# Kernel tuning notes

Measured on AMD Instinct MI355X. Metric: run time of the kernel, lower is better.

## Reference

```python
import jax, jax.numpy as jnp
from jax import lax
import numpy as np

B, C, H, W = 8, 256, 64, 64
DSTATE, DCONV, EXPAND = 16, 4, 2
DI = EXPAND * C          # 512 d_inner
DTR = (C + 15) // 16     # 16 dt_rank = ceil(d_model/16)

# ---------- helpers ----------

def _ln(x, g, b):
    m = x.mean(-1, keepdims=True)
    v = x.var(-1, keepdims=True)
    return (x - m) * lax.rsqrt(v + 1e-5) * g + b


def _bn(x, g, b):  # BatchNorm2d, training-mode batch stats
    m = x.mean((0, 2, 3), keepdims=True)
    v = x.var((0, 2, 3), keepdims=True)
    return (x - m) * lax.rsqrt(v + 1e-5) * g[None, :, None, None] + b[None, :, None, None]


def _gn(x, g, b, groups=32):
    Bb, Cc, Hh, Ww = x.shape
    xr = x.reshape(Bb, groups, Cc // groups, Hh, Ww)
    m = xr.mean((2, 3, 4), keepdims=True)
    v = xr.var((2, 3, 4), keepdims=True)
    xr = (xr - m) * lax.rsqrt(v + 1e-5)
    return xr.reshape(Bb, Cc, Hh, Ww) * g[None, :, None, None] + b[None, :, None, None]


def _hsig(x):  # h_sigmoid: relu6(x+3)/6
    return jnp.clip(x + 3.0, 0.0, 6.0) / 6.0


def _axial(v, idx, pos):
    # v: [B,C,N]; pos: [1,C,16] linearly resized to N (align_corners=False == half-pixel)
    N = v.shape[-1]
    pe = jax.image.resize(pos, (1, pos.shape[1], N), method='linear')
    return v + pe + idx  # idx interpolation is identity (same size)


def _dwconvT(x, w):
    # ConvTranspose2d(k=3, stride=2, pad=1, out_pad=1, groups=C) == lhs-dilated corr with flipped kernel
    wf = w[:, :, ::-1, ::-1]
    return lax.conv_general_dilated(x, wf, window_strides=(1, 1), padding=((1, 2), (1, 2)),
                                    lhs_dilation=(2, 2), dimension_numbers=('NCHW', 'OIHW', 'NCHW'),
                                    feature_group_count=x.shape[1])


def _mamba(h, in_w, conv_w, conv_b, xproj_w, dt_w, dt_b, Alog, Dp, out_w):
    # standard mamba_ssm Mamba block forward; h: [B,L,d_model]
    Bb, L, _ = h.shape
    di = in_w.shape[0] // 2
    N = Alog.shape[1]
    dtr = dt_w.shape[1]
    xz = h @ in_w.T                      # [B,L,2*di]
    xm, zg = xz[..., :di], xz[..., di:]
    # causal depthwise conv1d (pad K-1 left == torch pad both + slice [:L])
    xc = lax.conv_general_dilated(xm.transpose(0, 2, 1), conv_w, (1,), [(conv_w.shape[2] - 1, 0)],
                                  dimension_numbers=('NCH', 'OIH', 'NCH'), feature_group_count=di)
    u = jax.nn.silu(xc + conv_b[None, :, None]).transpose(0, 2, 1)  # [B,L,di]
    dbl = u @ xproj_w.T                  # [B,L,dtr+2N]
    dt = jax.nn.softplus(dbl[..., :dtr] @ dt_w.T + dt_b)            # [B,L,di]
    Bm = dbl[..., dtr:dtr + N]
    Cm = dbl[..., dtr + N:]
    A = -jnp.exp(Alog)                   # [di,N]
    dA = jnp.exp(dt[..., None] * A)      # [B,L,di,N]
    dBu = (dt * u)[..., None] * Bm[:, :, None, :]

    def step(hst, inp):
        dA_t, dBu_t = inp
        hst = dA_t * hst + dBu_t
        return hst, hst

    h0 = jnp.zeros((Bb, di, N), dt.dtype)
    _, hs = lax.scan(step, h0, (dA.transpose(1, 0, 2, 3), dBu.transpose(1, 0, 2, 3)))
    y = jnp.einsum('lbdn,bln->bld', hs, Cm) + Dp * u
    y = y * jax.nn.silu(zg)
    return y @ out_w.T


def _forward(x, pos_embed, ln_w, ln_b, proj_w, proj_b,
             up_dw_w, up_bn1_g, up_bn1_b, up_pw_w, up_bn2_g, up_bn2_b,
             down_pw_w, down_bn_g, down_bn_b, gn_g, gn_b,
             f_in_w, f_conv_w, f_conv_b, f_xproj_w, f_dt_w, f_dt_b, f_Alog, f_D, f_out_w,
             b_in_w, b_conv_w, b_conv_b, b_xproj_w, b_dt_w, b_dt_b, b_Alog, b_D, b_out_w):
    # upsample branch: dwconvT -> BN -> ReLU -> 1x1 -> BN -> ReLU6
    z = _dwconvT(x, up_dw_w)
    z = jax.nn.relu(_bn(z, up_bn1_g, up_bn1_b))
    z = jnp.einsum('oc,bchw->bohw', up_pw_w, z)
    z = jnp.clip(_bn(z, up_bn2_g, up_bn2_b), 0.0, 6.0)  # act1 = ReLU6
    dt = x.dtype
    col_max = _ln(_axial(x.max(2), jnp.argmax(x, 2).astype(dt), pos_embed).transpose(0, 2, 1), ln_w, ln_b)
    col_min = _ln(_axial(x.min(2), jnp.argmin(x, 2).astype(dt), pos_embed).transpose(0, 2, 1), ln_w, ln_b)
    row_max = _ln(_axial(x.max(3), jnp.argmax(x, 3).astype(dt), pos_embed).transpose(0, 2, 1), ln_w, ln_b)
    row_min = _ln(_axial(x.min(3), jnp.argmin(x, 3).astype(dt), pos_embed).transpose(0, 2, 1), ln_w, ln_b)
    result_max = jnp.concatenate([col_max, row_max], 1)  # [B, W+H, C]
    result_min = jnp.concatenate([col_min, row_min], 1)
    fpar = (f_in_w, f_conv_w, f_conv_b, f_xproj_w, f_dt_w, f_dt_b, f_Alog, f_D, f_out_w)
    bpar = (b_in_w, b_conv_w, b_conv_b, b_xproj_w, b_dt_w, b_dt_b, b_Alog, b_D, b_out_w)
    fmax = _ln(_mamba(result_max, *fpar), ln_w, ln_b)
    fmin = _ln(_mamba(result_min, *fpar), ln_w, ln_b)
    bmax = _ln(_mamba(jnp.flip(result_max, 1), *bpar), ln_w, ln_b)
    bmin = _ln(_mamba(jnp.flip(result_min, 1), *bpar), ln_w, ln_b)
    res_max = jnp.concatenate([fmax, jnp.flip(bmax, 1)], -1) @ proj_w.T + proj_b
    res_max = _ln(res_max, ln_w, ln_b)
    res_min = jnp.concatenate([fmin, jnp.flip(bmin, 1)], -1) @ proj_w.T + proj_b
    res_min = _ln(res_min, ln_w, ln_b)
    res = res_max[:, :, None, :] + res_min[:, None, :, :]  # [B,L,L,C], L=H+W
    res = res.transpose(0, 3, 1, 2)                        # [B,C,L,L] == [B,C,2H,2W]
    res = _hsig(res) * z
    res = _gn(res, gn_g, gn_b)
    res = jnp.einsum('oc,bchw->bohw', down_pw_w, res[:, :, ::2, ::2])  # 1x1 stride-2 conv
    res = _bn(res, down_bn_g, down_bn_b)
    res = _gn(res, gn_g, gn_b)
    res = res + x
    res = _gn(res, gn_g, gn_b)
    return res


def setup_inputs() -> dict:
    key = jax.random.key(0)
    ks = jax.random.split(key, 32)

    def n(i, shape, s=0.02):
        return jax.random.normal(ks[i], shape, jnp.float32) * s

    inp = {}
    inp['x'] = jax.random.normal(ks[0], (B, C, H, W), jnp.float32)
    inp['pos_embed'] = jax.random.normal(ks[1], (1, C, 16), jnp.float32)
    inp['ln_w'] = jnp.ones((C,), jnp.float32)
    inp['ln_b'] = jnp.zeros((C,), jnp.float32)
    inp['proj_w'] = n(2, (C, 2 * C))
    inp['proj_b'] = jnp.zeros((C,), jnp.float32)
    inp['up_dw_w'] = n(3, (C, 1, 3, 3), 0.1)
    inp['up_bn1_g'] = jnp.ones((C,), jnp.float32)
    inp['up_bn1_b'] = jnp.zeros((C,), jnp.float32)
    inp['up_pw_w'] = n(4, (C, C), 0.05)
    inp['up_bn2_g'] = jnp.ones((C,), jnp.float32)
    inp['up_bn2_b'] = jnp.zeros((C,), jnp.float32)
    inp['down_pw_w'] = n(5, (C, C), 0.05)
    inp['down_bn_g'] = jnp.ones((C,), jnp.float32)
    inp['down_bn_b'] = jnp.zeros((C,), jnp.float32)
    inp['gn_g'] = jnp.ones((C,), jnp.float32)
    inp['gn_b'] = jnp.zeros((C,), jnp.float32)
    Alog = jnp.tile(jnp.log(jnp.arange(1, DSTATE + 1, dtype=jnp.float32))[None, :], (DI, 1))
    dtb = jnp.full((DI,), float(np.log(np.expm1(0.01))), jnp.float32)
    for p, k0 in (('f', 6), ('b', 16)):
        inp[p + '_in_w'] = n(k0, (2 * DI, C))
        inp[p + '_conv_w'] = n(k0 + 1, (DI, 1, DCONV), 0.2)
        inp[p + '_conv_b'] = jnp.zeros((DI,), jnp.float32)
        inp[p + '_xproj_w'] = n(k0 + 2, (DTR + 2 * DSTATE, DI))
        inp[p + '_dt_w'] = n(k0 + 3, (DI, DTR), 0.1)
        inp[p + '_dt_b'] = dtb
        inp[p + '_Alog'] = Alog
        inp[p + '_D'] = jnp.ones((DI,), jnp.float32)
        inp[p + '_out_w'] = n(k0 + 4, (C, DI))
    return inp


def reference(x, pos_embed, ln_w, ln_b, proj_w, proj_b,
              up_dw_w, up_bn1_g, up_bn1_b, up_pw_w, up_bn2_g, up_bn2_b,
              down_pw_w, down_bn_g, down_bn_b, gn_g, gn_b,
              f_in_w, f_conv_w, f_conv_b, f_xproj_w, f_dt_w, f_dt_b, f_Alog, f_D, f_out_w,
              b_in_w, b_conv_w, b_conv_b, b_xproj_w, b_dt_w, b_dt_b, b_Alog, b_D, b_out_w):
    return _forward(x, pos_embed, ln_w, ln_b, proj_w, proj_b,
                    up_dw_w, up_bn1_g, up_bn1_b, up_pw_w, up_bn2_g, up_bn2_b,
                    down_pw_w, down_bn_g, down_bn_b, gn_g, gn_b,
                    f_in_w, f_conv_w, f_conv_b, f_xproj_w, f_dt_w, f_dt_b, f_Alog, f_D, f_out_w,
                    b_in_w, b_conv_w, b_conv_b, b_xproj_w, b_dt_w, b_dt_b, b_Alog, b_D, b_out_w)
```

## Files before the change

### kernel.cpp

```cpp
#include <hip/hip_runtime.h>
#include <hip/hip_bf16.h>

typedef __hip_bfloat16 bf16;
typedef __attribute__((ext_vector_type(8))) short bf16x8v;
typedef __attribute__((ext_vector_type(4))) short bf16x4v;
typedef __attribute__((ext_vector_type(4))) float f32x4v;

#define B_ 8
#define C_ 256
#define L_ 128
#define MB 1048576UL

__device__ inline float b2f(bf16 v){ return __bfloat162float(v); }
__device__ inline bf16 f2b(float v){ return __float2bfloat16(v); }
__device__ inline short b2s(bf16 v){ return *(short*)&v; }
__device__ inline float siluf(float x){ return x / (1.f + expf(-x)); }
__device__ inline float softplusf(float x){ return (x > 20.f) ? x : log1pf(expf(x)); }
__device__ inline float vclamp(float v){ return fmaxf(v, 0.f) + 1e-5f; }

__device__ inline void bred2(float& a, float& b, float* red){
  #pragma unroll
  for (int m = 1; m < 64; m <<= 1){ a += __shfl_xor(a, m); b += __shfl_xor(b, m); }
  int tid = threadIdx.x, wave = tid >> 6, lane = tid & 63;
  __syncthreads();
  if (lane == 0){ red[wave] = a; red[8 + wave] = b; }
  __syncthreads();
  a = red[0] + red[1] + red[2] + red[3];
  b = red[8] + red[9] + red[10] + red[11];
}

__device__ inline int tswz(int p, int c){
  return (p*512 + c*2) ^ (((p ^ (p >> 2)) & 7) << 4);
}

__global__ __launch_bounds__(64) void pool1_kernel(const float* __restrict__ x, const float* __restrict__ pos,
    float* __restrict__ pcolmax, float* __restrict__ pcolmin,
    float* __restrict__ prowmax, float* __restrict__ prowmin, float* __restrict__ sxb)
{
  int c = blockIdx.x, b = blockIdx.y, t = threadIdx.x;
  __shared__ float xs[64][65];
  const float* xp = x + ((long)(b*C_ + c))*4096;
  for (int i = 0; i < 64; i++) xs[i][t] = xp[i*64 + t];
  __syncthreads();
  float tt = 0.25f*(float)t - 0.375f;
  const float* pp = pos + c*16;
  float pe;
  if (tt <= 0.f) pe = pp[0];
  else if (tt >= 15.f) pe = pp[15];
  else { int f = (int)floorf(tt); float w = tt - (float)f; pe = pp[f]*(1.f - w) + pp[f+1]*w; }
  float vmax = -1e30f, vmin = 1e30f; int amax = 0, amin = 0;
  for (int j = 0; j < 64; j++){
    float v = xs[t][j];
    if (v > vmax){ vmax = v; amax = j; }
    if (v < vmin){ vmin = v; amin = j; }
  }
  long o = (long)(b*64 + t)*C_ + c;
  prowmax[o] = vmax + pe + (float)amax;
  prowmin[o] = vmin + pe + (float)amin;
  vmax = -1e30f; vmin = 1e30f; amax = 0; amin = 0;
  float sx = 0.f, sx2 = 0.f;
  for (int i = 0; i < 64; i++){
    float v = xs[i][t];
    if (v > vmax){ vmax = v; amax = i; }
    if (v < vmin){ vmin = v; amin = i; }
    sx += v; sx2 += v*v;
  }
  pcolmax[o] = vmax + pe + (float)amax;
  pcolmin[o] = vmin + pe + (float)amin;
  #pragma unroll
  for (int m = 1; m < 64; m <<= 1){ sx += __shfl_xor(sx, m); sx2 += __shfl_xor(sx2, m); }
  if (t == 0){ sxb[(b << 8) + c] = sx; sxb[2048 + (b << 8) + c] = sx2; }
}

__global__ __launch_bounds__(256) void pool2_kernel(const float* __restrict__ pcolmax, const float* __restrict__ pcolmin,
    const float* __restrict__ prowmax, const float* __restrict__ prowmin,
    const float* __restrict__ lnw, const float* __restrict__ lnb, bf16* __restrict__ hbuf)
{
  int r = blockIdx.x, b = blockIdx.y, c = threadIdx.x;
  __shared__ float red[16];
  int p = r & 63;
  long src = (long)(b*64 + p)*C_ + c;
  float vmax = (r < 64) ? pcolmax[src] : prowmax[src];
  float vmin = (r < 64) ? pcolmin[src] : prowmin[src];
  float gw = lnw[c], gb = lnb[c];
  long row = (long)b*L_ + r, frow = (long)b*L_ + (127 - r);
  float s = vmax, s2 = vmax*vmax;
  bred2(s, s2, red);
  float m = s*(1.f/256.f), var = s2*(1.f/256.f) - m*m;
  float o = (vmax - m)*rsqrtf(vclamp(var))*gw + gb;
  hbuf[0*262144 + row*C_ + c]  = f2b(o);
  hbuf[2*262144 + frow*C_ + c] = f2b(o);
  s = vmin; s2 = vmin*vmin;
  bred2(s, s2, red);
  m = s*(1.f/256.f); var = s2*(1.f/256.f) - m*m;
  o = (vmin - m)*rsqrtf(vclamp(var))*gw + gb;
  hbuf[1*262144 + row*C_ + c]  = f2b(o);
  hbuf[3*262144 + frow*C_ + c] = f2b(o);
}

__global__ __launch_bounds__(256) void dwz1_kernel(const float* __restrict__ x, const float* __restrict__ dw,
    bf16* __restrict__ z1, float* __restrict__ bn1sum, float* __restrict__ bn1sq)
{
  int bc = blockIdx.x; int c = bc & 255;
  int tid = threadIdx.x;
  __shared__ float xs[4096];
  const float* xp = x + (long)bc*4096;
  for (int it = 0; it < 16; it++) xs[it*256 + tid] = xp[it*256 + tid];
  float w[9];
  #pragma unroll
  for (int q = 0; q < 9; q++) w[q] = dw[c*9 + q];
  __syncthreads();
  bf16* zp = z1 + (long)bc*16384;
  float s = 0.f, s2 = 0.f;
  for (int it = 0; it < 64; it++){
    int p = it*256 + tid; int i = p >> 7, j = p & 127;
    int xi = i >> 1, xj = j >> 1;
    int io = i & 1, jo = j & 1;
    int xi1 = (xi < 63) ? xi + 1 : 63;
    int xj1 = (xj < 63) ? xj + 1 : 63;
    float XA = xs[xi*64 + xj];
    float XB = xs[xi*64 + xj1];
    float XC = xs[xi1*64 + xj];
    float XD = xs[xi1*64 + xj1];
    float wA = jo ? (io ? w[8] : w[5]) : (io ? w[7] : w[4]);
    float wB = (jo && j < 127) ? (io ? w[6] : w[3]) : 0.f;
    float wC = (io && i < 127) ? (jo ? w[2] : w[1]) : 0.f;
    float wD = (io && jo && i < 127 && j < 127) ? w[0] : 0.f;
    float acc = wA*XA;
    acc += wB*XB;
    acc += wC*XC;
    acc += wD*XD;
    zp[p] = f2b(acc);
    s += acc; s2 += acc*acc;
  }
  __shared__ float red[16];
  bred2(s, s2, red);
  if (tid == 0){ atomicAdd(&bn1sum[c], s); atomicAdd(&bn1sq[c], s2); }
}

__global__ __launch_bounds__(256) void wcvt_all_kernel(
    const float* __restrict__ s0, const float* __restrict__ s1, const float* __restrict__ s2,
    const float* __restrict__ s3, const float* __restrict__ s4, const float* __restrict__ s5,
    const float* __restrict__ s6, const float* __restrict__ s7, const float* __restrict__ s8,
    bf16* __restrict__ d0, bf16* __restrict__ d1, bf16* __restrict__ d2,
    bf16* __restrict__ d3, bf16* __restrict__ d4, bf16* __restrict__ d5,
    bf16* __restrict__ d6, bf16* __restrict__ d7, bf16* __restrict__ d8)
{
  int seg = blockIdx.y;
  const float* s; bf16* d; int n;
  switch (seg){
    case 0: s = s0; d = d0; n = 262144; break;
    case 1: s = s1; d = d1; n = 262144; break;
    case 2: s = s2; d = d2; n = 24576;  break;
    case 3: s = s3; d = d3; n = 24576;  break;
    case 4: s = s4; d = d4; n = 131072; break;
    case 5: s = s5; d = d5; n = 131072; break;
    case 6: s = s6; d = d6; n = 131072; break;
    case 7: s = s7; d = d7; n = 65536;  break;
    default: s = s8; d = d8; n = 65536; break;
  }
  long i = ((long)blockIdx.x*256 + threadIdx.x)*4;
  if (i >= n) return;
  float4 v = *(const float4*)&s[i];
  bf16 o[4] = {f2b(v.x), f2b(v.y), f2b(v.z), f2b(v.w)};
  *(uint2*)&d[i] = *(const uint2*)o;
}

__global__ __launch_bounds__(256) void pwz_fused_kernel(const bf16* __restrict__ z1,
    const float* __restrict__ bn1sum, const float* __restrict__ bn1sq,
    const float* __restrict__ g1, const float* __restrict__ b1,
    const bf16* __restrict__ Wb, bf16* __restrict__ z2,
    float* __restrict__ bn2part)
{
  int b = blockIdx.y;
  int p0 = blockIdx.x*64;
  int tid = threadIdx.x;
  __shared__ __align__(16) short Tb[16384];
  {
    int pc = tid & 15, ch = tid >> 4;
    #pragma unroll
    for (int it = 0; it < 8; it++){
      int c = (ch + it*16)*2;
      const bf16* r0 = &z1[((long)(b*C_ + c))*16384 + p0 + pc*4];
      bf16x4v va = *(const bf16x4v*)r0;
      bf16x4v vb = *(const bf16x4v*)(r0 + 16384);
      float m0v = bn1sum[c]*(1.f/131072.f);
      float v0 = bn1sq[c]*(1.f/131072.f) - m0v*m0v;
      float a0 = g1[c]*rsqrtf(vclamp(v0));
      float d0 = b1[c] - m0v*a0;
      float m1v = bn1sum[c+1]*(1.f/131072.f);
      float v1 = bn1sq[c+1]*(1.f/131072.f) - m1v*m1v;
      float a1 = g1[c+1]*rsqrtf(vclamp(v1));
      float d1 = b1[c+1] - m1v*a1;
      #pragma unroll
      for (int k = 0; k < 4; k++){
        int p = pc*4 + k;
        bf16 h0; *(short*)&h0 = va[k];
        bf16 h1; *(short*)&h1 = vb[k];
        bf16 o0 = f2b(fmaxf(b2f(h0)*a0 + d0, 0.f));
        bf16 o1 = f2b(fmaxf(b2f(h1)*a1 + d1, 0.f));
        unsigned int u = ((unsigned int)(*(unsigned short*)&o1) << 16) | (unsigned int)(*(unsigned short*)&o0);
        *(unsigned int*)((char*)Tb + tswz(p, c)) = u;
      }
    }
  }
  __syncthreads();
  int wave = tid >> 6, lane = tid & 63;
  int quad = lane >> 4, l16 = lane & 15;
  f32x4v acc[4][4];
  #pragma unroll
  for (int i = 0; i < 4; i++)
    #pragma unroll
    for (int j = 0; j < 4; j++) acc[i][j] = (f32x4v){0.f, 0.f, 0.f, 0.f};
  for (int k0 = 0; k0 < 256; k0 += 32){
    int c = k0 + quad*8;
    bf16x8v a[4], bb[4];
    #pragma unroll
    for (int ms = 0; ms < 4; ms++)
      a[ms] = *(const bf16x8v*)&Wb[(wave*64 + ms*16 + l16)*C_ + c];
    #pragma unroll
    for (int ns = 0; ns < 4; ns++){
      int p = ns*16 + l16;
      bb[ns] = *(const bf16x8v*)((const char*)Tb + tswz(p, c));
    }
    #pragma unroll
    for (int ms = 0; ms < 4; ms++)
      #pragma unroll
      for (int ns = 0; ns < 4; ns++)
        acc[ms][ns] = __builtin_amdgcn_mfma_f32_16x16x32_bf16(bb[ns], a[ms], acc[ms][ns], 0, 0, 0);
  }
  int slot = (blockIdx.x & 7) | (b << 3);
  #pragma unroll
  for (int ms = 0; ms < 4; ms++){
    int o = wave*64 + ms*16 + l16;
    long rowbase = ((long)(b*C_ + o))*16384 + p0;
    float s = 0.f, s2 = 0.f;
    #pragma unroll
    for (int ns = 0; ns < 4; ns++){
      bf16 ov[4];
      #pragma unroll
      for (int r = 0; r < 4; r++){
        bf16 bv = f2b(acc[ms][ns][r]);
        ov[r] = bv;
        float vv = b2f(bv);
        s += vv; s2 += vv*vv;
      }
      *(uint2*)&z2[rowbase + ns*16 + quad*4] = *(const uint2*)ov;
    }
    s += __shfl_xor(s, 16);  s += __shfl_xor(s, 32);
    s2 += __shfl_xor(s2, 16); s2 += __shfl_xor(s2, 32);
    if (quad == 0){
      atomicAdd(&bn2part[slot*256 + o], s);
      atomicAdd(&bn2part[16384 + slot*256 + o], s2);
    }
  }
}

__global__ __launch_bounds__(256) void inproj_mfma_kernel(const bf16* __restrict__ hb,
    const bf16* __restrict__ Wif, const bf16* __restrict__ Wib2, bf16* __restrict__ xz)
{
  int v = blockIdx.z;
  int m0 = blockIdx.y*256, n0 = blockIdx.x*64;
  const bf16* A = hb + (long)v*262144;
  const bf16* W = (v >= 2) ? Wib2 : Wif;
  bf16* out = xz + (long)v*1048576;
  int tid = threadIdx.x;
  int wave = tid >> 6, lane = tid & 63;
  int quad = lane >> 4, l16 = lane & 15;
  f32x4v acc[4][4];
  #pragma unroll
  for (int i = 0; i < 4; i++)
    #pragma unroll
    for (int j = 0; j < 4; j++) acc[i][j] = (f32x4v){0.f, 0.f, 0.f, 0.f};
  for (int k0 = 0; k0 < 256; k0 += 32){
    int c = k0 + quad*8;
    bf16x8v a[4], bb[4];
    #pragma unroll
    for (int ms = 0; ms < 4; ms++)
      a[ms] = *(const bf16x8v*)&A[(long)(m0 + wave*64 + ms*16 + l16)*256 + c];
    #pragma unroll
    for (int ns = 0; ns < 4; ns++)
      bb[ns] = *(const bf16x8v*)&W[(long)(n0 + ns*16 + l16)*256 + c];
    #pragma unroll
    for (int ms = 0; ms < 4; ms++)
      #pragma unroll
      for (int ns = 0; ns < 4; ns++)
        acc[ms][ns] = __builtin_amdgcn_mfma_f32_16x16x32_bf16(bb[ns], a[ms], acc[ms][ns], 0, 0, 0);
  }
  #pragma unroll
  for (int ms = 0; ms < 4; ms++){
    int m = m0 + wave*64 + ms*16 + l16;
    #pragma unroll
    for (int ns = 0; ns < 4; ns++){
      bf16 ov[4];
      #pragma unroll
      for (int r = 0; r < 4; r++) ov[r] = f2b(acc[ms][ns][r]);
      *(uint2*)&out[(long)m*1024 + n0 + ns*16 + quad*4] = *(const uint2*)ov;
    }
  }
}

__global__ __launch_bounds__(256) void xproj_mfma_kernel(const bf16* __restrict__ ub,
    const bf16* __restrict__ Wxf, const bf16* __restrict__ Wxb, float* __restrict__ dblb)
{
  int v = blockIdx.y;
  int m0 = blockIdx.x*256;
  const bf16* A = ub + (long)v*524288;
  const bf16* W = (v >= 2) ? Wxb : Wxf;
  float* out = dblb + (long)v*49152;
  int tid = threadIdx.x;
  int wave = tid >> 6, lane = tid & 63;
  int quad = lane >> 4, l16 = lane & 15;
  f32x4v acc[4][3];
  #pragma unroll
  for (int i = 0; i < 4; i++)
    #pragma unroll
    for (int j = 0; j < 3; j++) acc[i][j] = (f32x4v){0.f, 0.f, 0.f, 0.f};
  for (int k0 = 0; k0 < 512; k0 += 32){
    int c = k0 + quad*8;
    bf16x8v a[4], bb[3];
    #pragma unroll
    for (int ms = 0; ms < 4; ms++)
      a[ms] = *(const bf16x8v*)&A[(long)(m0 + wave*64 + ms*16 + l16)*512 + c];
    #pragma unroll
    for (int ns = 0; ns < 3; ns++)
      bb[ns] = *(const bf16x8v*)&W[(long)(ns*16 + l16)*512 + c];
    #pragma unroll
    for (int ms = 0; ms < 4; ms++)
      #pragma unroll
      for (int ns = 0; ns < 3; ns++)
        acc[ms][ns] = __builtin_amdgcn_mfma_f32_16x16x32_bf16(bb[ns], a[ms], acc[ms][ns], 0, 0, 0);
  }
  #pragma unroll
  for (int ms = 0; ms < 4; ms++){
    int m = m0 + wave*64 + ms*16 + l16;
    #pragma unroll
    for (int ns = 0; ns < 3; ns++)
      *(f32x4v*)&out[(long)m*48 + ns*16 + quad*4] = acc[ms][ns];
  }
}

__global__ __launch_bounds__(256) void outproj_mfma_kernel(const bf16* __restrict__ yb,
    const bf16* __restrict__ Wof, const bf16* __restrict__ Wob, float* __restrict__ mo)
{
  int v = blockIdx.z;
  int m0 = blockIdx.y*256, n0 = blockIdx.x*64;
  const bf16* A = yb + (long)v*524288;
  const bf16* W = (v >= 2) ? Wob : Wof;
  float* out = mo + (long)v*262144;
  int tid = threadIdx.x;
  int wave = tid >> 6, lane = tid & 63;
  int quad = lane >> 4, l16 = lane & 15;
  f32x4v acc[4][4];
  #pragma unroll
  for (int i = 0; i < 4; i++)
    #pragma unroll
    for (int j = 0; j < 4; j++) acc[i][j] = (f32x4v){0.f, 0.f, 0.f, 0.f};
  for (int k0 = 0; k0 < 512; k0 += 32){
    int c = k0 + quad*8;
    bf16x8v a[4], bb[4];
    #pragma unroll
    for (int ms = 0; ms < 4; ms++)
      a[ms] = *(const bf16x8v*)&A[(long)(m0 + wave*64 + ms*16 + l16)*512 + c];
    #pragma unroll
    for (int ns = 0; ns < 4; ns++)
      bb[ns] = *(const bf16x8v*)&W[(long)(n0 + ns*16 + l16)*512 + c];
    #pragma unroll
    for (int ms = 0; ms < 4; ms++)
      #pragma unroll
      for (int ns = 0; ns < 4; ns++)
        acc[ms][ns] = __builtin_amdgcn_mfma_f32_16x16x32_bf16(bb[ns], a[ms], acc[ms][ns], 0, 0, 0);
  }
  #pragma unroll
  for (int ms = 0; ms < 4; ms++){
    int m = m0 + wave*64 + ms*16 + l16;
    #pragma unroll
    for (int ns = 0; ns < 4; ns++)
      *(f32x4v*)&out[(long)m*256 + n0 + ns*16 + quad*4] = acc[ms][ns];
  }
}

__global__ __launch_bounds__(256) void pj_mfma_kernel(const bf16* __restrict__ cb,
    const bf16* __restrict__ Wp, const float* __restrict__ pb, float* __restrict__ rp)
{
  int z = blockIdx.z;
  int m0 = blockIdx.y*256, n0 = blockIdx.x*64;
  const bf16* A = cb + (long)z*524288;
  float* out = rp + (long)z*262144;
  int tid = threadIdx.x;
  int wave = tid >> 6, lane = tid & 63;
  int quad = lane >> 4, l16 = lane & 15;
  f32x4v acc[4][4];
  #pragma unroll
  for (int i = 0; i < 4; i++)
    #pragma unroll
    for (int j = 0; j < 4; j++) acc[i][j] = (f32x4v){0.f, 0.f, 0.f, 0.f};
  for (int k0 = 0; k0 < 512; k0 += 32){
    int c = k0 + quad*8;
    bf16x8v a[4], bb[4];
    #pragma unroll
    for (int ms = 0; ms < 4; ms++)
      a[ms] = *(const bf16x8v*)&A[(long)(m0 + wave*64 + ms*16 + l16)*512 + c];
    #pragma unroll
    for (int ns = 0; ns < 4; ns++)
      bb[ns] = *(const bf16x8v*)&Wp[(long)(n0 + ns*16 + l16)*512 + c];
    #pragma unroll
    for (int ms = 0; ms < 4; ms++)
      #pragma unroll
      for (int ns = 0; ns < 4; ns++)
        acc[ms][ns] = __builtin_amdgcn_mfma_f32_16x16x32_bf16(bb[ns], a[ms], acc[ms][ns], 0, 0, 0);
  }
  #pragma unroll
  for (int ns = 0; ns < 4; ns++){
    float4 pbv = *(const float4*)&pb[n0 + ns*16 + quad*4];
    #pragma unroll
    for (int ms = 0; ms < 4; ms++){
      int m = m0 + wave*64 + ms*16 + l16;
      f32x4v vv = acc[ms][ns];
      vv[0] += pbv.x; vv[1] += pbv.y; vv[2] += pbv.z; vv[3] += pbv.w;
      *(f32x4v*)&out[(long)m*256 + n0 + ns*16 + quad*4] = vv;
    }
  }
}

__global__ __launch_bounds__(256) void gemm_kernel(
  const float* __restrict__ Abase, long sA, int lda,
  const float* __restrict__ W0, const float* __restrict__ W1,
  const float* __restrict__ bias0, const float* __restrict__ bias1, int wsplit,
  float* __restrict__ Cbase, long sC, int ldc,
  int M, int N, int K, int act)
{
  int z = blockIdx.z;
  const float* A = Abase + (long)z*sA;
  float* Cp = Cbase + (long)z*sC;
  const float* W = (z >= wsplit) ? W1 : W0;
  const float* bias = (z >= wsplit) ? bias1 : bias0;
  int m0 = blockIdx.y*64, n0 = blockIdx.x*64;
  __shared__ __align__(16) float As[16][68];
  __shared__ __align__(16) float Ws[16][68];
  int tid = threadIdx.x, tx = tid & 15, ty = tid >> 4;
  float acc[4][4] = {};
  for (int k0 = 0; k0 < K; k0 += 16){
    #pragma unroll
    for (int q = 0; q < 4; q++){
      int e = tid + q*256; int r = e >> 4, kk = e & 15;
      int mi = m0 + r, ki = k0 + kk;
      As[kk][r] = (mi < M && ki < K) ? A[(long)mi*lda + ki] : 0.f;
    }
    #pragma unroll
    for (int q = 0; q < 4; q++){
      int e = tid + q*256; int n = e >> 4, kk = e & 15;
      int ni = n0 + n, ki = k0 + kk;
      Ws[kk][n] = (ni < N && ki < K) ? W[(long)ni*K + ki] : 0.f;
    }
    __syncthreads();
    #pragma unroll
    for (int kk = 0; kk < 16; kk++){
      float4 a4 = *(const float4*)&As[kk][ty*4];
      float4 b4 = *(const float4*)&Ws[kk][tx*4];
      float av[4] = {a4.x, a4.y, a4.z, a4.w};
      float bv[4] = {b4.x, b4.y, b4.z, b4.w};
      #pragma unroll
      for (int mm = 0; mm < 4; mm++)
        #pragma unroll
        for (int nn = 0; nn < 4; nn++) acc[mm][nn] += av[mm]*bv[nn];
    }
    __syncthreads();
  }
  #pragma unroll
  for (int mm = 0; mm < 4; mm++){
    int mi = m0 + ty*4 + mm;
    if (mi >= M) continue;
    #pragma unroll
    for (int nn = 0; nn < 4; nn++){
      int ni = n0 + tx*4 + nn;
      if (ni >= N) continue;
      float v = acc[mm][nn];
      if (bias) v += bias[ni];
      if (act == 2) v = softplusf(v);
      Cp[(long)mi*ldc + ni] = v;
    }
  }
}

__global__ __launch_bounds__(512) void conv1d_kernel(const bf16* __restrict__ xzb,
    const float* __restrict__ fw, const float* __restrict__ fb,
    const float* __restrict__ bw, const float* __restrict__ bb,
    bf16* __restrict__ ub)
{
  int l = blockIdx.x, b = blockIdx.y, v = blockIdx.z, d = threadIdx.x;
  const bf16* xm = xzb + (long)v*1024*1024;
  const float* w  = (v < 2) ? fw : bw;
  const float* cb = (v < 2) ? fb : bb;
  float acc = cb[d];
  #pragma unroll
  for (int k = 0; k < 4; k++){
    int ll = l - 3 + k;
    if (ll >= 0) acc += b2f(xm[(long)(b*L_ + ll)*1024 + d]) * w[d*4 + k];
  }
  ub[(long)v*1024*512 + (long)(b*L_ + l)*512 + d] = f2b(siluf(acc));
}

__global__ __launch_bounds__(64) void scan_kernel(const float* __restrict__ dtb, const bf16* __restrict__ ub,
    const float* __restrict__ dblb, const bf16* __restrict__ xzb,
    const float* __restrict__ fAlog, const float* __restrict__ fD,
    const float* __restrict__ bAlog, const float* __restrict__ bD,
    bf16* __restrict__ yb)
{
  int v = blockIdx.z, b = blockIdx.y;
  int tid = threadIdx.x;
  int dd = tid & 15, qtr = tid >> 4;
  int d0 = blockIdx.x*16;
  int d = d0 + dd;
  const float* dt  = dtb  + (long)v*1024*512;
  const bf16*  u   = ub   + (long)v*1024*512;
  const float* dbl = dblb + (long)v*1024*48;
  const bf16*  zg  = xzb  + (long)v*1024*1024 + 512;
  const float* Alog = (v < 2) ? fAlog : bAlog;
  const float* Dp   = (v < 2) ? fD : bD;
  __shared__ __align__(16) short sdt[16][136];
  __shared__ __align__(16) short su_[16][136];
  __shared__ __align__(16) short szg[16][136];
  __shared__ __align__(16) short sB [16][136];
  __shared__ __align__(16) short sC [16][136];
  long row = (long)b*L_;
  for (int idx = tid; idx < 2048; idx += 64){
    int l = idx >> 4, j = idx & 15;
    sdt[j][l] = b2s(f2b(dt[(row + l)*512 + d0 + j]));
    su_[j][l] = b2s(u[(row + l)*512 + d0 + j]);
    szg[j][l] = b2s(zg[(row + l)*1024 + d0 + j]);
    sB [j][l] = b2s(f2b(dbl[(row + l)*48 + 16 + j]));
    sC [j][l] = b2s(f2b(dbl[(row + l)*48 + 32 + j]));
  }
  float a2[4];
  #pragma unroll
  for (int n = 0; n < 4; n++) a2[n] = -expf(Alog[d*16 + qtr*4 + n]) * 1.44269504f;
  float Dv = Dp[d];
  float h[4];
  #pragma unroll
  for (int n = 0; n < 4; n++) h[n] = 0.f;
  __syncthreads();
  bf16* yo = yb + (long)v*1024*512;
  for (int l0 = 0; l0 < 128; l0 += 8){
    bf16x8v dt8 = *(const bf16x8v*)&sdt[dd][l0];
    bf16x8v u8  = *(const bf16x8v*)&su_[dd][l0];
    bf16x8v zg8 = *(const bf16x8v*)&szg[dd][l0];
    bf16x8v B8[4], C8[4];
    #pragma unroll
    for (int n = 0; n < 4; n++){
      B8[n] = *(const bf16x8v*)&sB[qtr*4 + n][l0];
      C8[n] = *(const bf16x8v*)&sC[qtr*4 + n][l0];
    }
    #pragma unroll
    for (int k = 0; k < 8; k++){
      bf16 t0; *(short*)&t0 = dt8[k]; float dtv = b2f(t0);
      bf16 t1; *(short*)&t1 = u8[k];  float uv  = b2f(t1);
      bf16 t2; *(short*)&t2 = zg8[k]; float zgv = b2f(t2);
      float dtu = dtv*uv;
      float acc = 0.f;
      #pragma unroll
      for (int n = 0; n < 4; n++){
        float dA = exp2f(dtv*a2[n]);
        bf16 tb; *(short*)&tb = B8[n][k];
        bf16 tc; *(short*)&tc = C8[n][k];
        h[n] = dA*h[n] + dtu*b2f(tb);
        acc += h[n]*b2f(tc);
      }
      acc += __shfl_xor(acc, 16);
      acc += __shfl_xor(acc, 32);
      if (qtr == 0)
        yo[(row + l0 + k)*512 + d] = f2b((acc + Dv*uv) * siluf(zgv));
    }
  }
}

__global__ __launch_bounds__(256) void ln_kernel(const float* __restrict__ inb, bf16* __restrict__ outb0,
    bf16* __restrict__ outb1, float* __restrict__ outf,
    const float* __restrict__ lnw, const float* __restrict__ lnb, int mode)
{
  int r = blockIdx.x, b = blockIdx.y, v = blockIdx.z, c = threadIdx.x;
  long row = (long)b*L_ + r;
  float val = inb[((long)v*1024 + row)*C_ + c];
  __shared__ float red[16];
  float s = val, s2 = val*val;
  bred2(s, s2, red);
  float m = s*(1.f/256.f), var = s2*(1.f/256.f) - m*m;
  float o = (val - m)*rsqrtf(vclamp(var))*lnw[c] + lnb[c];
  if (mode == 1){
    long frow = (long)b*L_ + (127 - r);
    if (v == 0)      outb0[row*512 + c] = f2b(o);
    else if (v == 1) outb1[row*512 + c] = f2b(o);
    else if (v == 2) outb0[frow*512 + 256 + c] = f2b(o);
    else             outb1[frow*512 + 256 + c] = f2b(o);
  } else {
    outf[((long)v*1024 + row)*C_ + c] = o;
  }
}

__global__ __launch_bounds__(256) void hsig_kernel(bf16* __restrict__ z2, const float* __restrict__ rm,
    const float* __restrict__ rn, const float* __restrict__ bn2part,
    const float* __restrict__ g2, const float* __restrict__ b2,
    float* __restrict__ gnsum, float* __restrict__ gnsq)
{
  int c = blockIdx.x, b = blockIdx.y, tid = threadIdx.x;
  __shared__ float red[16];
  __shared__ float rms[128], rns[128];
  if (tid < 128){
    rms[tid] = rm[(long)(b*L_ + tid)*C_ + c];
    rns[tid] = rn[(long)(b*L_ + tid)*C_ + c];
  }
  float pa = 0.f, pb = 0.f;
  if (tid < 64){ pa = bn2part[tid*256 + c]; pb = bn2part[16384 + tid*256 + c]; }
  bred2(pa, pb, red);
  float mm2 = pa*(1.f/131072.f);
  float vv2 = pb*(1.f/131072.f) - mm2*mm2;
  float aa = g2[c] * rsqrtf(vclamp(vv2));
  float dd = b2[c] - mm2*aa;
  bf16* zp = z2 + ((long)(b*C_ + c))*16384;
  float pre[16];
  #pragma unroll
  for (int g = 0; g < 4; g++)
    #pragma unroll
    for (int q = 0; q < 4; q++)
      pre[g*4 + q] = b2f(zp[g*1024 + q*256 + tid]);
  __syncthreads();
  float s = 0.f, s2 = 0.f;
  #pragma unroll
  for (int g = 0; g < 4; g++){
    #pragma unroll
    for (int q = 0; q < 4; q++){
      int p = g*1024 + q*256 + tid; int i = p >> 7, j = p & 127;
      float zv = pre[g*4 + q]*aa + dd;
      zv = fminf(fmaxf(zv, 0.f), 6.f);
      float gate = rms[i] + rns[j];
      gate = fminf(fmaxf(gate + 3.f, 0.f), 6.f) * (1.f/6.f);
      float t = gate*zv;
      s += t; s2 += t*t;
      if (((i | j) & 1) == 0) zp[(i >> 1)*64 + (j >> 1)] = f2b(t);
    }
  }
  for (int g = 4; g < 16; g++){
    #pragma unroll
    for (int q = 0; q < 4; q++){
      int p = g*1024 + q*256 + tid; int i = p >> 7, j = p & 127;
      float zv = b2f(zp[p])*aa + dd;
      zv = fminf(fmaxf(zv, 0.f), 6.f);
      float gate = rms[i] + rns[j];
      gate = fminf(fmaxf(gate + 3.f, 0.f), 6.f) * (1.f/6.f);
      float t = gate*zv;
      s += t; s2 += t*t;
      if (((i | j) & 1) == 0) zp[(i >> 1)*64 + (j >> 1)] = f2b(t);
    }
  }
  bred2(s, s2, red);
  if (tid == 0){ atomicAdd(&gnsum[b*32 + (c >> 3)], s); atomicAdd(&gnsq[b*32 + (c >> 3)], s2); }
}

__global__ __launch_bounds__(256) void pwdown_fused_kernel(const bf16* __restrict__ z2,
    const float* __restrict__ gnsum, const float* __restrict__ gnsq,
    const float* __restrict__ gn_g, const float* __restrict__ gn_b,
    const bf16* __restrict__ Wb, const float* __restrict__ x,
    float* __restrict__ out, float* __restrict__ sds)
{
  int b = blockIdx.y;
  int p0 = blockIdx.x*64;
  int tid = threadIdx.x;
  __shared__ __align__(16) short Tb[16384];
  {
    int pc = tid & 15, ch = tid >> 4;
    #pragma unroll
    for (int it = 0; it < 8; it++){
      int c = (ch + it*16)*2;
      const bf16* r0 = &z2[((long)(b*C_ + c))*16384 + p0 + pc*4];
      bf16x4v va = *(const bf16x4v*)r0;
      bf16x4v vb = *(const bf16x4v*)(r0 + 16384);
      float m0v = gnsum[b*32 + (c >> 3)]*(1.f/131072.f);
      float v0 = gnsq[b*32 + (c >> 3)]*(1.f/131072.f) - m0v*m0v;
      float iv = rsqrtf(vclamp(v0));
      float a0 = iv*gn_g[c],   d0 = gn_b[c]   - m0v*(iv*gn_g[c]);
      float a1 = iv*gn_g[c+1], d1 = gn_b[c+1] - m0v*(iv*gn_g[c+1]);
      #pragma unroll
      for (int k = 0; k < 4; k++){
        int p = pc*4 + k;
        bf16 h0; *(short*)&h0 = va[k];
        bf16 h1; *(short*)&h1 = vb[k];
        bf16 o0 = f2b(b2f(h0)*a0 + d0);
        bf16 o1 = f2b(b2f(h1)*a1 + d1);
        unsigned int u = ((unsigned int)(*(unsigned short*)&o1) << 16) | (unsigned int)(*(unsigned short*)&o0);
        *(unsigned int*)((char*)Tb + tswz(p, c)) = u;
      }
    }
  }
  __syncthreads();
  int wave = tid >> 6, lane = tid & 63;
  int quad = lane >> 4, l16 = lane & 15;
  f32x4v acc[4][4];
  #pragma unroll
  for (int i = 0; i < 4; i++)
    #pragma unroll
    for (int j = 0; j < 4; j++) acc[i][j] = (f32x4v){0.f, 0.f, 0.f, 0.f};
  for (int k0 = 0; k0 < 256; k0 += 32){
    int c = k0 + quad*8;
    bf16x8v a[4], bb[4];
    #pragma unroll
    for (int ms = 0; ms < 4; ms++)
      a[ms] = *(const bf16x8v*)&Wb[(wave*64 + ms*16 + l16)*C_ + c];
    #pragma unroll
    for (int ns = 0; ns < 4; ns++){
      int p = ns*16 + l16;
      bb[ns] = *(const bf16x8v*)((const char*)Tb + tswz(p, c));
    }
    #pragma unroll
    for (int ms = 0; ms < 4; ms++)
      #pragma unroll
      for (int ns = 0; ns < 4; ns++)
        acc[ms][ns] = __builtin_amdgcn_mfma_f32_16x16x32_bf16(bb[ns], a[ms], acc[ms][ns], 0, 0, 0);
  }
  #pragma unroll
  for (int ms = 0; ms < 4; ms++){
    int o = wave*64 + ms*16 + l16;
    long rowbase = ((long)(b*C_ + o))*4096 + p0;
    float sd = 0.f, sd2 = 0.f, sdx = 0.f;
    #pragma unroll
    for (int ns = 0; ns < 4; ns++){
      f32x4v v4 = acc[ms][ns];
      long base = rowbase + ns*16 + quad*4;
      *(f32x4v*)&out[base] = v4;
      float4 xv = *(const float4*)&x[base];
      sd += v4[0] + v4[1] + v4[2] + v4[3];
      sd2 += v4[0]*v4[0] + v4[1]*v4[1] + v4[2]*v4[2] + v4[3]*v4[3];
      sdx += v4[0]*xv.x + v4[1]*xv.y + v4[2]*xv.z + v4[3]*xv.w;
    }
    sd += __shfl_xor(sd, 16);  sd += __shfl_xor(sd, 32);
    sd2 += __shfl_xor(sd2, 16); sd2 += __shfl_xor(sd2, 32);
    sdx += __shfl_xor(sdx, 16); sdx += __shfl_xor(sdx, 32);
    if (quad == 0){
      int oc = (b << 8) + o;
      atomicAdd(&sds[oc], sd);
      atomicAdd(&sds[2048 + oc], sd2);
      atomicAdd(&sds[4096 + oc], sdx);
    }
  }
}

__global__ __launch_bounds__(256) void final_kernel(const float* __restrict__ x,
    const float* __restrict__ sds, const float* __restrict__ sxb,
    const float* __restrict__ dbn_g, const float* __restrict__ dbn_b,
    const float* __restrict__ gn_g, const float* __restrict__ gn_b,
    float* __restrict__ out)
{
  int c = blockIdx.x, b = blockIdx.y, tid = threadIdx.x;
  __shared__ float lv[11][8];
  int g8 = (c >> 3) << 3;
  if (tid < 8){
    int cc = g8 + tid;
    float sd = 0.f, sd2 = 0.f;
    for (int bb2 = 0; bb2 < 8; bb2++){ sd += sds[bb2*256 + cc]; sd2 += sds[2048 + bb2*256 + cc]; }
    float mB = sd*(1.f/32768.f);
    float vB = sd2*(1.f/32768.f) - mB*mB;
    float ab = dbn_g[cc] * rsqrtf(vclamp(vB));
    float db = dbn_b[cc] - mB*ab;
    float inv_n = 1.f/4096.f;
    float m = sds[b*256 + cc]*inv_n, Ed2 = sds[2048 + b*256 + cc]*inv_n;
    float mx = sxb[b*256 + cc]*inv_n, Ex2 = sxb[2048 + b*256 + cc]*inv_n;
    float Edx = sds[4096 + b*256 + cc]*inv_n;
    float Ev = ab*m + db;
    float Ev2 = ab*ab*Ed2 + 2.f*ab*db*m + db*db;
    lv[0][tid] = ab; lv[1][tid] = db; lv[2][tid] = m; lv[3][tid] = Ed2;
    lv[4][tid] = mx; lv[5][tid] = Ex2; lv[6][tid] = Edx; lv[7][tid] = Ev; lv[8][tid] = Ev2;
  }
  __syncthreads();
  if (tid < 8){
    float m1 = 0.f, q1 = 0.f;
    for (int k = 0; k < 8; k++){ m1 += lv[7][k]; q1 += lv[8][k]; }
    m1 *= 0.125f; q1 *= 0.125f;
    int cc = g8 + tid;
    float inv1 = rsqrtf(vclamp(q1 - m1*m1));
    float A1 = inv1*gn_g[cc];
    float D1 = gn_b[cc] - m1*A1;
    float ab = lv[0][tid], db = lv[1][tid];
    float m = lv[2][tid], Ed2 = lv[3][tid], mx = lv[4][tid], Ex2 = lv[5][tid], Edx = lv[6][tid];
    float al = A1*ab;
    float be = A1*db + D1;
    float Et = al*m + be + mx;
    float Et2 = al*al*Ed2 + 2.f*al*be*m + be*be + 2.f*al*Edx + 2.f*be*mx + Ex2;
    lv[9][tid] = Et; lv[10][tid] = Et2; lv[0][tid] = al; lv[1][tid] = be;
  }
  __syncthreads();
  float m2 = 0.f, q2 = 0.f;
  for (int k = 0; k < 8; k++){ m2 += lv[9][k]; q2 += lv[10][k]; }
  m2 *= 0.125f; q2 *= 0.125f;
  float G = rsqrtf(vclamp(q2 - m2*m2))*gn_g[c];
  float P = G*lv[0][c & 7];
  float Q = G;
  float R = G*(lv[1][c & 7] - m2) + gn_b[c];
  long base = ((long)(b*C_ + c))*4096;
  for (int it = 0; it < 16; it++){
    long idx = base + it*256 + tid;
    out[idx] = P*out[idx] + Q*x[idx] + R;
  }
}

extern "C" void kernel_launch(void* const* d_in, const int* in_sizes, int n_in,
                              void* d_out, int out_size, void* d_ws, size_t ws_size,
                              hipStream_t stream)
{
  (void)in_sizes; (void)n_in; (void)out_size; (void)ws_size;
  const float* x         = (const float*)d_in[0];
  const float* pos       = (const float*)d_in[1];
  const float* ln_w      = (const float*)d_in[2];
  const float* ln_b      = (const float*)d_in[3];
  const float* proj_w    = (const float*)d_in[4];
  const float* proj_b    = (const float*)d_in[5];
  const float* up_dw_w   = (const float*)d_in[6];
  const float* up_bn1_g  = (const float*)d_in[7];
  const float* up_bn1_b  = (const float*)d_in[8];
  const float* up_pw_w   = (const float*)d_in[9];
  const float* up_bn2_g  = (const float*)d_in[10];
  const float* up_bn2_b  = (const float*)d_in[11];
  const float* down_pw_w = (const float*)d_in[12];
  const float* down_bn_g = (const float*)d_in[13];
  const float* down_bn_b = (const float*)d_in[14];
  const float* gn_g      = (const float*)d_in[15];
  const float* gn_b      = (const float*)d_in[16];
  const float* f_in_w    = (const float*)d_in[17];
  const float* f_conv_w  = (const float*)d_in[18];
  const float* f_conv_b  = (const float*)d_in[19];
  const float* f_xproj_w = (const float*)d_in[20];
  const float* f_dt_w    = (const float*)d_in[21];
  const float* f_dt_b    = (const float*)d_in[22];
  const float* f_Alog    = (const float*)d_in[23];
  const float* f_D       = (const float*)d_in[24];
  const float* f_out_w   = (const float*)d_in[25];
  const float* b_in_w    = (const float*)d_in[26];
  const float* b_conv_w  = (const float*)d_in[27];
  const float* b_conv_b  = (const float*)d_in[28];
  const float* b_xproj_w = (const float*)d_in[29];
  const float* b_dt_w    = (const float*)d_in[30];
  const float* b_dt_b    = (const float*)d_in[31];
  const float* b_Alog    = (const float*)d_in[32];
  const float* b_D       = (const float*)d_in[33];
  const float* b_out_w   = (const float*)d_in[34];

  char* sb = (char*)d_ws;
  float* statz  = (float*)(sb);
  float* sds    = (float*)(sb + 6144);
  float* bn2part= (float*)(sb + 32768);
  float* sxb    = (float*)(sb + 184320);
  float* rmrn  = (float*)(sb + 1*MB);
  bf16*  Wbbuf = (bf16*)(sb + 3*MB);
  bf16*  Wb2buf= (bf16*)(sb + 3*MB + 262144);
  bf16*  Wpb   = (bf16*)(sb + 3*MB + 524288);
  char* big = sb + 4*MB;
  float* pool4  = (float*)(big + 0*MB);
  bf16*  hbufb  = (bf16*)(big + 2*MB);
  bf16*  Wif    = (bf16*)(big + 4*MB);
  bf16*  Wib2   = (bf16*)(big + 4*MB + 524288);
  bf16*  Wxf    = (bf16*)(big + 5*MB);
  bf16*  Wxb    = (bf16*)(big + 5*MB + 65536);
  bf16*  Wof    = (bf16*)(big + 5*MB + 131072);
  bf16*  Wob    = (bf16*)(big + 5*MB + 393216);
  bf16*  xzbuf  = (bf16*)(big + 6*MB);
  bf16*  ubuf   = (bf16*)(big + 22*MB);
  float* dblbuf = (float*)(big + 30*MB);
  float* dtbuf  = (float*)(big + 31*MB);
  bf16*  ybuf   = (bf16*)(big + 39*MB);
  float* mout   = (float*)(big + 47*MB);
  bf16*  cbufb  = (bf16*)(big + 51*MB);
  float* respre = (float*)(big + 55*MB);
  bf16*  z1buf  = (bf16*)(big);
  bf16*  z2buf  = (bf16*)(big);
  float* dbuf   = (float*)d_out;

  float* bn1sum = statz;        float* bn1sq = statz + 256;
  float* gnsum  = statz + 1024; float* gnsq  = statz + 1280;
  float* pcolmax = pool4;
  float* pcolmin = pool4 + 131072;
  float* prowmax = pool4 + 262144;
  float* prowmin = pool4 + 393216;

  hipMemsetAsync(statz, 0, 163840, stream);

  wcvt_all_kernel<<<dim3(256, 9), 256, 0, stream>>>(
      f_in_w, b_in_w, f_xproj_w, b_xproj_w, f_out_w, b_out_w, proj_w, up_pw_w, down_pw_w,
      Wif, Wib2, Wxf, Wxb, Wof, Wob, Wpb, Wbbuf, Wb2buf);

  pool1_kernel<<<dim3(256, 8), 64, 0, stream>>>(x, pos, pcolmax, pcolmin, prowmax, prowmin, sxb);
  pool2_kernel<<<dim3(128, 8), 256, 0, stream>>>(pcolmax, pcolmin, prowmax, prowmin, ln_w, ln_b, hbufb);
  inproj_mfma_kernel<<<dim3(16, 4, 4), 256, 0, stream>>>(hbufb, Wif, Wib2, xzbuf);
  conv1d_kernel<<<dim3(128, 8, 4), 512, 0, stream>>>(xzbuf, f_conv_w, f_conv_b, b_conv_w, b_conv_b, ubuf);
  xproj_mfma_kernel<<<dim3(4, 4), 256, 0, stream>>>(ubuf, Wxf, Wxb, dblbuf);
  gemm_kernel<<<dim3(8, 16, 4), 256, 0, stream>>>(dblbuf, 49152, 48, f_dt_w, b_dt_w, f_dt_b, b_dt_b, 2,
                                                  dtbuf, 524288, 512, 1024, 512, 16, 2);
  scan_kernel<<<dim3(32, 8, 4), 64, 0, stream>>>(dtbuf, ubuf, dblbuf, xzbuf, f_Alog, f_D, b_Alog, b_D, ybuf);
  outproj_mfma_kernel<<<dim3(4, 4, 4), 256, 0, stream>>>(ybuf, Wof, Wob, mout);
  ln_kernel<<<dim3(128, 8, 4), 256, 0, stream>>>(mout, cbufb, cbufb + 524288, nullptr, ln_w, ln_b, 1);
  pj_mfma_kernel<<<dim3(4, 4, 2), 256, 0, stream>>>(cbufb, Wpb, proj_b, respre);
  ln_kernel<<<dim3(128, 8, 2), 256, 0, stream>>>(respre, nullptr, nullptr, rmrn, ln_w, ln_b, 0);

  dwz1_kernel<<<2048, 256, 0, stream>>>(x, up_dw_w, z1buf, bn1sum, bn1sq);
  pwz_fused_kernel<<<dim3(256, 8), 256, 0, stream>>>(z1buf, bn1sum, bn1sq, up_bn1_g, up_bn1_b,
                                                     Wbbuf, z2buf, bn2part);

  hsig_kernel<<<dim3(256, 8), 256, 0, stream>>>(z2buf, rmrn, rmrn + 262144, bn2part,
                                                up_bn2_g, up_bn2_b, gnsum, gnsq);
  pwdown_fused_kernel<<<dim3(64, 8), 256, 0, stream>>>(z2buf, gnsum, gnsq, gn_g, gn_b,
                                                       Wb2buf, x, dbuf, sds);
  final_kernel<<<dim3(256, 8), 256, 0, stream>>>(x, sds, sxb, down_bn_g, down_bn_b, gn_g, gn_b,
                                                 (float*)d_out);
}
```

Measured before the change: 483.5 us.

## Vectorize global loads, precompute norm coefficients in shared memory, store dt as bf16

Several unrelated micro-optimizations. The pool1, dwz1 and final kernels now use float4 global loads and stores instead of scalar ones. The pwz and pwdown kernels compute per-channel BN/GN scale and shift once per block into shared memory rather than redundantly per thread. The dt GEMM gains a mode that writes softplus output as bf16, halving dt traffic, and the scan reads it directly. The dt rounding point is unchanged, since scan previously converted dt to bf16 anyway.

```diff
diff --git a/kernel.cpp b/kernel.cpp
--- a/kernel.cpp
+++ b/kernel.cpp
@@ -40,7 +40,14 @@
   int c = blockIdx.x, b = blockIdx.y, t = threadIdx.x;
   __shared__ float xs[64][65];
   const float* xp = x + ((long)(b*C_ + c))*4096;
-  for (int i = 0; i < 64; i++) xs[i][t] = xp[i*64 + t];
+  const float4* xp4 = (const float4*)xp;
+  #pragma unroll
+  for (int q = 0; q < 16; q++){
+    float4 v = xp4[q*64 + t];
+    int e = q*64 + t;
+    int i = e >> 4, cc = (e & 15) << 2;
+    xs[i][cc] = v.x; xs[i][cc+1] = v.y; xs[i][cc+2] = v.z; xs[i][cc+3] = v.w;
+  }
   __syncthreads();
   float tt = 0.25f*(float)t - 0.375f;
   const float* pp = pos + c*16;
@@ -103,9 +110,11 @@
 {
   int bc = blockIdx.x; int c = bc & 255;
   int tid = threadIdx.x;
-  __shared__ float xs[4096];
-  const float* xp = x + (long)bc*4096;
-  for (int it = 0; it < 16; it++) xs[it*256 + tid] = xp[it*256 + tid];
+  __shared__ __align__(16) float xs[4096];
+  const float4* xp4 = (const float4*)(x + (long)bc*4096);
+  #pragma unroll
+  for (int q = 0; q < 4; q++)
+    *(float4*)&xs[(q*256 + tid)*4] = xp4[q*256 + tid];
   float w[9];
   #pragma unroll
   for (int q = 0; q < 9; q++) w[q] = dw[c*9 + q];
@@ -176,6 +185,14 @@
   int p0 = blockIdx.x*64;
   int tid = threadIdx.x;
   __shared__ __align__(16) short Tb[16384];
+  __shared__ float aa[256], dd[256];
+  {
+    float m = bn1sum[tid]*(1.f/131072.f);
+    float v = bn1sq[tid]*(1.f/131072.f) - m*m;
+    float a = g1[tid]*rsqrtf(vclamp(v));
+    aa[tid] = a; dd[tid] = b1[tid] - m*a;
+  }
+  __syncthreads();
   {
     int pc = tid & 15, ch = tid >> 4;
     #pragma unroll
@@ -184,14 +201,7 @@
       const bf16* r0 = &z1[((long)(b*C_ + c))*16384 + p0 + pc*4];
       bf16x4v va = *(const bf16x4v*)r0;
       bf16x4v vb = *(const bf16x4v*)(r0 + 16384);
-      float m0v = bn1sum[c]*(1.f/131072.f);
-      float v0 = bn1sq[c]*(1.f/131072.f) - m0v*m0v;
-      float a0 = g1[c]*rsqrtf(vclamp(v0));
-      float d0 = b1[c] - m0v*a0;
-      float m1v = bn1sum[c+1]*(1.f/131072.f);
-      float v1 = bn1sq[c+1]*(1.f/131072.f) - m1v*m1v;
-      float a1 = g1[c+1]*rsqrtf(vclamp(v1));
-      float d1 = b1[c+1] - m1v*a1;
+      float a0 = aa[c], d0 = dd[c], a1 = aa[c+1], d1 = dd[c+1];
       #pragma unroll
       for (int k = 0; k < 4; k++){
         int p = pc*4 + k;
@@ -432,7 +442,6 @@
 {
   int z = blockIdx.z;
   const float* A = Abase + (long)z*sA;
-  float* Cp = Cbase + (long)z*sC;
   const float* W = (z >= wsplit) ? W1 : W0;
   const float* bias = (z >= wsplit) ? bias1 : bias0;
   int m0 = blockIdx.y*64, n0 = blockIdx.x*64;
@@ -477,8 +486,14 @@
       if (ni >= N) continue;
       float v = acc[mm][nn];
       if (bias) v += bias[ni];
-      if (act == 2) v = softplusf(v);
-      Cp[(long)mi*ldc + ni] = v;
+      if (act >= 2) v = softplusf(v);
+      if (act == 3){
+        bf16* Cb = (bf16*)Cbase + (long)z*sC;
+        Cb[(long)mi*ldc + ni] = f2b(v);
+      } else {
+        float* Cp = Cbase + (long)z*sC;
+        Cp[(long)mi*ldc + ni] = v;
+      }
     }
   }
 }
@@ -501,7 +516,7 @@
   ub[(long)v*1024*512 + (long)(b*L_ + l)*512 + d] = f2b(siluf(acc));
 }
 
-__global__ __launch_bounds__(64) void scan_kernel(const float* __restrict__ dtb, const bf16* __restrict__ ub,
+__global__ __launch_bounds__(64) void scan_kernel(const bf16* __restrict__ dtb, const bf16* __restrict__ ub,
     const float* __restrict__ dblb, const bf16* __restrict__ xzb,
     const float* __restrict__ fAlog, const float* __restrict__ fD,
     const float* __restrict__ bAlog, const float* __restrict__ bD,
@@ -512,7 +527,7 @@
   int dd = tid & 15, qtr = tid >> 4;
   int d0 = blockIdx.x*16;
   int d = d0 + dd;
-  const float* dt  = dtb  + (long)v*1024*512;
+  const bf16*  dt  = dtb  + (long)v*1024*512;
   const bf16*  u   = ub   + (long)v*1024*512;
   const float* dbl = dblb + (long)v*1024*48;
   const bf16*  zg  = xzb  + (long)v*1024*1024 + 512;
@@ -526,7 +541,7 @@
   long row = (long)b*L_;
   for (int idx = tid; idx < 2048; idx += 64){
     int l = idx >> 4, j = idx & 15;
-    sdt[j][l] = b2s(f2b(dt[(row + l)*512 + d0 + j]));
+    sdt[j][l] = b2s(dt[(row + l)*512 + d0 + j]);
     su_[j][l] = b2s(u[(row + l)*512 + d0 + j]);
     szg[j][l] = b2s(zg[(row + l)*1024 + d0 + j]);
     sB [j][l] = b2s(f2b(dbl[(row + l)*48 + 16 + j]));
@@ -666,6 +681,14 @@
   int p0 = blockIdx.x*64;
   int tid = threadIdx.x;
   __shared__ __align__(16) short Tb[16384];
+  __shared__ float gA[256], gD[256];
+  {
+    float m = gnsum[b*32 + (tid >> 3)]*(1.f/131072.f);
+    float v = gnsq[b*32 + (tid >> 3)]*(1.f/131072.f) - m*m;
+    float A = rsqrtf(vclamp(v))*gn_g[tid];
+    gA[tid] = A; gD[tid] = gn_b[tid] - m*A;
+  }
+  __syncthreads();
   {
     int pc = tid & 15, ch = tid >> 4;
     #pragma unroll
@@ -674,11 +697,8 @@
       const bf16* r0 = &z2[((long)(b*C_ + c))*16384 + p0 + pc*4];
       bf16x4v va = *(const bf16x4v*)r0;
       bf16x4v vb = *(const bf16x4v*)(r0 + 16384);
-      float m0v = gnsum[b*32 + (c >> 3)]*(1.f/131072.f);
-      float v0 = gnsq[b*32 + (c >> 3)]*(1.f/131072.f) - m0v*m0v;
-      float iv = rsqrtf(vclamp(v0));
-      float a0 = iv*gn_g[c],   d0 = gn_b[c]   - m0v*(iv*gn_g[c]);
-      float a1 = iv*gn_g[c+1], d1 = gn_b[c+1] - m0v*(iv*gn_g[c+1]);
+      float a0 = gA[c], d0 = gD[c];
+      float a1 = gA[c + 1], d1 = gD[c + 1];
       #pragma unroll
       for (int k = 0; k < 4; k++){
         int p = pc*4 + k;
@@ -794,10 +814,19 @@
   float P = G*lv[0][c & 7];
   float Q = G;
   float R = G*(lv[1][c & 7] - m2) + gn_b[c];
-  long base = ((long)(b*C_ + c))*4096;
-  for (int it = 0; it < 16; it++){
+  long base = ((long)(b*C_ + c))*1024;
+  const float4* x4 = (const float4*)x;
+  float4* o4 = (float4*)out;
+  #pragma unroll
+  for (int it = 0; it < 4; it++){
     long idx = base + it*256 + tid;
-    out[idx] = P*out[idx] + Q*x[idx] + R;
+    float4 o = o4[idx];
+    float4 xv = x4[idx];
+    o.x = P*o.x + Q*xv.x + R;
+    o.y = P*o.y + Q*xv.y + R;
+    o.z = P*o.z + Q*xv.z + R;
+    o.w = P*o.w + Q*xv.w + R;
+    o4[idx] = o;
   }
 }
 
@@ -863,7 +892,7 @@
   bf16*  xzbuf  = (bf16*)(big + 6*MB);
   bf16*  ubuf   = (bf16*)(big + 22*MB);
   float* dblbuf = (float*)(big + 30*MB);
-  float* dtbuf  = (float*)(big + 31*MB);
+  bf16*  dtbuf  = (bf16*)(big + 31*MB);
   bf16*  ybuf   = (bf16*)(big + 39*MB);
   float* mout   = (float*)(big + 47*MB);
   bf16*  cbufb  = (bf16*)(big + 51*MB);
@@ -891,7 +920,7 @@
   conv1d_kernel<<<dim3(128, 8, 4), 512, 0, stream>>>(xzbuf, f_conv_w, f_conv_b, b_conv_w, b_conv_b, ubuf);
   xproj_mfma_kernel<<<dim3(4, 4), 256, 0, stream>>>(ubuf, Wxf, Wxb, dblbuf);
   gemm_kernel<<<dim3(8, 16, 4), 256, 0, stream>>>(dblbuf, 49152, 48, f_dt_w, b_dt_w, f_dt_b, b_dt_b, 2,
-                                                  dtbuf, 524288, 512, 1024, 512, 16, 2);
+                                                  (float*)dtbuf, 524288, 512, 1024, 512, 16, 3);
   scan_kernel<<<dim3(32, 8, 4), 64, 0, stream>>>(dtbuf, ubuf, dblbuf, xzbuf, f_Alog, f_D, b_Alog, b_D, ybuf);
   outproj_mfma_kernel<<<dim3(4, 4, 4), 256, 0, stream>>>(ybuf, Wof, Wob, mout);
   ln_kernel<<<dim3(128, 8, 4), 256, 0, stream>>>(mout, cbufb, cbufb + 524288, nullptr, ln_w, ln_b, 1);
```

Measured after the change: 486.7 us. No clear change (+0.7%).
